# Kernel tuning notes

Hardware: AMD Instinct MI355X
Metric: run time of the kernel (lower is better)

## Reference

```python
import jax, jax.numpy as jnp
import numpy as np

N, IN_DIM, OUT_DIM = 8192, 1024, 1024

def setup_inputs() -> dict:
    key = jax.random.key(0)
    k1, k2, k3, k4 = jax.random.split(key, 4)
    return {
        "input_feature": jax.random.normal(k1, (N, IN_DIM), dtype=jnp.float32),
        "wq": jax.random.normal(k2, (IN_DIM, OUT_DIM), dtype=jnp.float32),
        "wk": jax.random.normal(k3, (IN_DIM, OUT_DIM), dtype=jnp.float32),
        "wv": jax.random.normal(k4, (IN_DIM, OUT_DIM), dtype=jnp.float32),
    }

def reference(input_feature, wq, wk, wv):
    # QKV projections: [N, out_dim]
    q = input_feature @ wq
    k = input_feature @ wk
    v = input_feature @ wv
    # Attention scores [N, N]; note: original applies NO 1/sqrt(d) scaling
    scores = q @ k.T
    attn = jax.nn.softmax(scores, axis=1)
    return attn @ v
```

## Files before the change

### kernel.cpp

```cpp
#include <hip/hip_runtime.h>
#include <hip/hip_bf16.h>
#include <math.h>

#define NROWS 8192
#define DIM   1024
#define CAP   256
#define MARGIN 120.0f

using f16x8 = __attribute__((ext_vector_type(8))) _Float16;
using f32x4 = __attribute__((ext_vector_type(4))) float;
typedef unsigned short u16;
typedef unsigned int   u32;

#define AS1 __attribute__((address_space(1)))
#define AS3 __attribute__((address_space(3)))

__global__ __launch_bounds__(256) void split2h(const float* __restrict__ X,
                                               u16* __restrict__ H,
                                               u16* __restrict__ L) {
    const int idx = (blockIdx.x * 256 + threadIdx.x) * 4;
    float4 x = *(const float4*)&X[idx];
    float c[4] = {x.x, x.y, x.z, x.w};
    u16 h[4], l[4];
#pragma unroll
    for (int i = 0; i < 4; ++i) {
        _Float16 hh = (_Float16)c[i];
        float r = c[i] - (float)hh;
        _Float16 ll = (_Float16)r;
        h[i] = *(u16*)&hh; l[i] = *(u16*)&ll;
    }
    *(ushort4*)&H[idx] = make_ushort4(h[0], h[1], h[2], h[3]);
    *(ushort4*)&L[idx] = make_ushort4(l[0], l[1], l[2], l[3]);
}

__global__ __launch_bounds__(256) void split_wvt(const float* __restrict__ W,
                                                 u16* __restrict__ H) {
    __shared__ float t[64][65];
    const int k0 = blockIdx.x * 64, n0 = blockIdx.y * 64;
    const int c = threadIdx.x & 63, r4 = threadIdx.x >> 6;
#pragma unroll
    for (int i = 0; i < 16; ++i) {
        int k = r4 + i * 4;
        t[k][c] = W[(size_t)(k0 + k) * DIM + n0 + c];
    }
    __syncthreads();
#pragma unroll
    for (int i = 0; i < 16; ++i) {
        int n = r4 + i * 4;
        _Float16 hb = (_Float16)t[c][n];
        H[(n0 + n) * DIM + k0 + c] = *(u16*)&hb;
    }
}

template<int NP>
__device__ __forceinline__ void gemm_lds(const u16* const (&Ap)[NP],
                                         const u16* const (&Bp)[NP],
                                         int row0, int col0, f32x4 (&acc)[4][4],
                                         short (&As)[2][2][4096], short (&Bs)[2][2][4096]) {
    const int tid = threadIdx.x;
    const int w = tid >> 6, lane = tid & 63;
    const int wy = w >> 1, wx = w & 1;
    const int quad = lane >> 4, r16 = lane & 15;

    const int    srow   = w * 32 + (lane >> 2);
    const int    schunk = (lane & 3) * 8;
    const size_t gA0 = (size_t)(row0 + srow) * DIM + schunk;
    const size_t gA1 = gA0 + (size_t)16 * DIM;
    const size_t gB0 = (size_t)(col0 + srow) * DIM + schunk;
    const size_t gB1 = gB0 + (size_t)16 * DIM;
    const int lds0 = (w * 32) * 32;
    const int lds1 = (w * 32 + 16) * 32;

    auto issue = [&](const u16* A, const u16* B, size_t k0, int buf) {
#pragma unroll
        for (int s = 0; s < 2; ++s) {
            const size_t ko = k0 + (size_t)s * 32;
            __builtin_amdgcn_global_load_lds((const AS1 u32*)(A + gA0 + ko), (AS3 u32*)&As[buf][s][lds0], 16, 0, 0);
            __builtin_amdgcn_global_load_lds((const AS1 u32*)(A + gA1 + ko), (AS3 u32*)&As[buf][s][lds1], 16, 0, 0);
            __builtin_amdgcn_global_load_lds((const AS1 u32*)(B + gB0 + ko), (AS3 u32*)&Bs[buf][s][lds0], 16, 0, 0);
            __builtin_amdgcn_global_load_lds((const AS1 u32*)(B + gB1 + ko), (AS3 u32*)&Bs[buf][s][lds1], 16, 0, 0);
        }
    };

    issue(Ap[0], Bp[0], 0, 0);

    int pp = 0;
#pragma unroll
    for (int p = 0; p < NP; ++p) {
        const u16* A = Ap[p];
        const u16* B = Bp[p];
        const u16* An = (p + 1 < NP) ? Ap[p + 1] : A;
        const u16* Bn = (p + 1 < NP) ? Bp[p + 1] : B;
        const bool more = (p + 1 < NP);
        for (int i = 0; i < 16; ++i) {
            __syncthreads();
            const int cur = pp, nxt = pp ^ 1;
            if (i < 15)      issue(A, B, (size_t)(i + 1) * 64, nxt);
            else if (more)   issue(An, Bn, 0, nxt);
#pragma unroll
            for (int s = 0; s < 2; ++s) {
                const short* AsC = As[cur][s];
                const short* BsC = Bs[cur][s];
                f16x8 af[4], bfr[4];
#pragma unroll
                for (int m = 0; m < 4; ++m)
                    af[m] = *(const f16x8*)&AsC[(wy * 64 + m * 16 + r16) * 32 + quad * 8];
#pragma unroll
                for (int n = 0; n < 4; ++n)
                    bfr[n] = *(const f16x8*)&BsC[(wx * 64 + n * 16 + r16) * 32 + quad * 8];
#pragma unroll
                for (int m = 0; m < 4; ++m)
#pragma unroll
                    for (int n = 0; n < 4; ++n)
                        acc[m][n] = __builtin_amdgcn_mfma_f32_16x16x32_f16(af[m], bfr[n], acc[m][n], 0, 0, 0);
            }
            pp ^= 1;
        }
    }
}

__global__ __launch_bounds__(256) void g_gemm(const u16* __restrict__ Wkh, const u16* __restrict__ Wkl,
                                              const u16* __restrict__ Wqh, const u16* __restrict__ Wql,
                                              float* __restrict__ Gt) {
    __shared__ short As[2][2][4096], Bs[2][2][4096];
    const int tid = threadIdx.x, w = tid >> 6, lane = tid & 63;
    const int wy = w >> 1, wx = w & 1, quad = lane >> 4, r16 = lane & 15;
    const int row0 = blockIdx.y * 128, col0 = blockIdx.x * 128;
    const u16* const Ap[3] = { Wkl, Wkh, Wkh };
    const u16* const Bp[3] = { Wqh, Wql, Wqh };
    f32x4 acc[4][4] = {};
    gemm_lds<3>(Ap, Bp, row0, col0, acc, As, Bs);
#pragma unroll
    for (int m = 0; m < 4; ++m)
#pragma unroll
        for (int n = 0; n < 4; ++n)
#pragma unroll
            for (int reg = 0; reg < 4; ++reg) {
                const int row = row0 + wy * 64 + m * 16 + quad * 4 + reg;
                const int col = col0 + wx * 64 + n * 16 + r16;
                Gt[row * DIM + col] = acc[m][n][reg];
            }
}

__global__ __launch_bounds__(256) void yv_gemm(const u16* __restrict__ Xh, const u16* __restrict__ Xl,
                                               const u16* __restrict__ Gth, const u16* __restrict__ Gtl,
                                               const u16* __restrict__ Wvth,
                                               float* __restrict__ Y, u16* __restrict__ Yh, u16* __restrict__ Vh) {
    __shared__ short As[2][2][4096], Bs[2][2][4096];
    const int tid = threadIdx.x, w = tid >> 6, lane = tid & 63;
    const int wy = w >> 1, wx = w & 1, quad = lane >> 4, r16 = lane & 15;
    const int id = blockIdx.x;
    const int z = id >> 9;
    const int within = id & 511;
    const int colt = within >> 6;
    const int rowt = within & 63;
    const int row0 = rowt * 128, col0 = colt * 128;
    f32x4 acc[4][4] = {};
    if (z == 0) {
        const u16* const Ap[3] = { Xl,  Xh,  Xh  };
        const u16* const Bp[3] = { Gth, Gtl, Gth };
        gemm_lds<3>(Ap, Bp, row0, col0, acc, As, Bs);
#pragma unroll
        for (int m = 0; m < 4; ++m)
#pragma unroll
            for (int n = 0; n < 4; ++n)
#pragma unroll
                for (int reg = 0; reg < 4; ++reg) {
                    const int row = row0 + wy * 64 + m * 16 + quad * 4 + reg;
                    const int col = col0 + wx * 64 + n * 16 + r16;
                    float v = acc[m][n][reg];
                    Y[row * DIM + col] = v;
                    _Float16 hb = (_Float16)v;
                    Yh[row * DIM + col] = *(u16*)&hb;
                }
    } else {
        const u16* const Ap[1] = { Xh };
        const u16* const Bp[1] = { Wvth };
        gemm_lds<1>(Ap, Bp, row0, col0, acc, As, Bs);
#pragma unroll
        for (int m = 0; m < 4; ++m)
#pragma unroll
            for (int n = 0; n < 4; ++n)
#pragma unroll
                for (int reg = 0; reg < 4; ++reg) {
                    const int row = row0 + wy * 64 + m * 16 + quad * 4 + reg;
                    const int col = col0 + wx * 64 + n * 16 + r16;
                    _Float16 hb = (_Float16)acc[m][n][reg];
                    Vh[row * DIM + col] = *(u16*)&hb;
                }
    }
}

__global__ __launch_bounds__(256) void filter_kernel(const u16* __restrict__ Yhp,
                                                     const u16* __restrict__ Xhp,
                                                     int* __restrict__ cnt,
                                                     int2* __restrict__ cand) {
    __shared__ short As[2][2][4096], Bs[2][2][4096];
    const int tid = threadIdx.x, w = tid >> 6, lane = tid & 63;
    const int wy = w >> 1, wx = w & 1, quad = lane >> 4, r16 = lane & 15;
    const int id = blockIdx.x;
    const int colt = id >> 6;
    const int rowt = id & 63;
    const int row0 = rowt * 128, col0 = colt * 128;

    const u16* const Ap[1] = { Yhp };
    const u16* const Bp[1] = { Xhp };
    f32x4 acc[4][4] = {};
    gemm_lds<1>(Ap, Bp, row0, col0, acc, As, Bs);

#pragma unroll
    for (int m = 0; m < 4; ++m) {
#pragma unroll
        for (int reg = 0; reg < 4; ++reg) {
            float mx = fmaxf(fmaxf(acc[m][0][reg], acc[m][1][reg]),
                             fmaxf(acc[m][2][reg], acc[m][3][reg]));
            mx = fmaxf(mx, __shfl_xor(mx, 1, 64));
            mx = fmaxf(mx, __shfl_xor(mx, 2, 64));
            mx = fmaxf(mx, __shfl_xor(mx, 4, 64));
            mx = fmaxf(mx, __shfl_xor(mx, 8, 64));
            const float th = mx - MARGIN;
            const int row = row0 + wy * 64 + m * 16 + quad * 4 + reg;
#pragma unroll
            for (int n = 0; n < 4; ++n) {
                float s = acc[m][n][reg];
                if (s >= th) {
                    int pos = atomicAdd(&cnt[row], 1);
                    if (pos < CAP)
                        cand[(size_t)row * CAP + pos] =
                            make_int2(col0 + wx * 64 + n * 16 + r16, __float_as_int(s));
                }
            }
        }
    }
}

__global__ __launch_bounds__(256) void finalize_kernel(const float* __restrict__ Y,
                                                       const float* __restrict__ X,
                                                       const u16* __restrict__ Vh,
                                                       const int* __restrict__ cnt,
                                                       const int2* __restrict__ cand,
                                                       float* __restrict__ out) {
    const int i = blockIdx.x;
    const int tid = threadIdx.x;
    const int w = tid >> 6, lane = tid & 63;
    __shared__ float  red[256];
    __shared__ int    surv[64];
    __shared__ double sprec[64];
    __shared__ float  wgt[64];
    __shared__ int    nsurv;

    const int c = min(cnt[i], CAP);
    float m = -3.0e38f;
    for (int t = tid; t < c; t += 256)
        m = fmaxf(m, __int_as_float(cand[(size_t)i * CAP + t].y));
    red[tid] = m;
    __syncthreads();
    for (int s = 128; s > 0; s >>= 1) {
        if (tid < s) red[tid] = fmaxf(red[tid], red[tid + s]);
        __syncthreads();
    }
    const float th = red[0] - MARGIN;
    if (tid == 0) nsurv = 0;
    __syncthreads();
    for (int t = tid; t < c; t += 256) {
        int2 e = cand[(size_t)i * CAP + t];
        if (__int_as_float(e.y) >= th) {
            int p = atomicAdd(&nsurv, 1);
            if (p < 64) surv[p] = e.x;
        }
    }
    __syncthreads();
    const int ns = min(nsurv, 64);
    for (int u = w; u < ns; u += 4) {
        const int j = surv[u];
        double a = 0.0;
        for (int d = lane; d < DIM; d += 64)
            a += (double)Y[(size_t)i * DIM + d] * (double)X[(size_t)j * DIM + d];
#pragma unroll
        for (int o = 32; o > 0; o >>= 1)
            a += __shfl_down(a, o, 64);
        if (lane == 0) sprec[u] = a;
    }
    __syncthreads();
    if (tid == 0) {
        double mm = -1.0e300;
        for (int u = 0; u < ns; ++u) mm = fmax(mm, sprec[u]);
        double l = 0.0;
        for (int u = 0; u < ns; ++u) l += exp(sprec[u] - mm);
        for (int u = 0; u < ns; ++u) wgt[u] = (float)(exp(sprec[u] - mm) / l);
    }
    __syncthreads();
    for (int d = tid; d < DIM; d += 256) {
        float o = 0.f;
        for (int u = 0; u < ns; ++u) {
            _Float16 hv = *(const _Float16*)&Vh[(size_t)surv[u] * DIM + d];
            o += wgt[u] * (float)hv;
        }
        out[(size_t)i * DIM + d] = o;
    }
}

extern "C" void kernel_launch(void* const* d_in, const int* in_sizes, int n_in,
                              void* d_out, int out_size, void* d_ws, size_t ws_size,
                              hipStream_t stream) {
    const float* X  = (const float*)d_in[0];
    const float* wq = (const float*)d_in[1];
    const float* wk = (const float*)d_in[2];
    const float* wv = (const float*)d_in[3];
    float* out = (float*)d_out;

    char* ws = (char*)d_ws;
    const size_t MB = 1024 * 1024;
    u16*   Xh   = (u16*)(ws +   0 * MB);
    u16*   Xl   = (u16*)(ws +  16 * MB);
    u16*   Wqh  = (u16*)(ws +  32 * MB);
    u16*   Wql  = (u16*)(ws +  34 * MB);
    u16*   Wkh  = (u16*)(ws +  36 * MB);
    u16*   Wkl  = (u16*)(ws +  38 * MB);
    u16*   Wvth = (u16*)(ws +  40 * MB);
    float* Gt   = (float*)(ws + 42 * MB);
    u16*   Gth  = (u16*)(ws +  46 * MB);
    u16*   Gtl  = (u16*)(ws +  48 * MB);
    float* Y    = (float*)(ws + 64 * MB);
    u16*   Yh   = (u16*)(ws +  96 * MB);
    u16*   Vh   = (u16*)(ws + 112 * MB);
    int*   cnt  = (int*)(ws + 128 * MB);
    int2*  cand = (int2*)(ws + 129 * MB);

    hipMemsetAsync(cnt, 0, (size_t)NROWS * 4, stream);

    split2h<<<NROWS * DIM / 1024, 256, 0, stream>>>(X, Xh, Xl);
    split2h<<<DIM * DIM / 1024, 256, 0, stream>>>(wq, Wqh, Wql);
    split2h<<<DIM * DIM / 1024, 256, 0, stream>>>(wk, Wkh, Wkl);
    split_wvt<<<dim3(16, 16), 256, 0, stream>>>(wv, Wvth);

    g_gemm<<<dim3(8, 8), 256, 0, stream>>>(Wkh, Wkl, Wqh, Wql, Gt);
    split2h<<<DIM * DIM / 1024, 256, 0, stream>>>(Gt, Gth, Gtl);

    yv_gemm<<<1024, 256, 0, stream>>>(Xh, Xl, Gth, Gtl, Wvth, Y, Yh, Vh);

    filter_kernel<<<4096, 256, 0, stream>>>(Yh, Xh, cnt, cand);

    finalize_kernel<<<NROWS, 256, 0, stream>>>(Y, X, Vh, cnt, cand, out);
}
```

Baseline: 645.4 us.

## Use 256x256 tiles with 4-stage async LDS pipeline for main GEMMs

```diff
diff --git a/kernel.cpp b/kernel.cpp
--- a/kernel.cpp
+++ b/kernel.cpp
@@ -119,6 +119,79 @@
     }
 }
 
+template<int NP>
+__device__ __forceinline__ void gemm256(const u16* const (&Ap)[NP],
+                                        const u16* const (&Bp)[NP],
+                                        int row0, int col0, f32x4 (&acc)[8][4],
+                                        short (&As)[4][8192], short (&Bs)[4][8192]) {
+    const int tid = threadIdx.x;
+    const int w = tid >> 6, lane = tid & 63;
+    const int wy = w >> 2, wx = w & 3;
+    const int quad = lane >> 4, r16 = lane & 15;
+
+    const int srow   = w * 16 + (lane >> 2);
+    const int schunk = ((lane & 3) ^ ((lane >> 3) & 3)) * 8;
+    const size_t gA0 = (size_t)(row0 + srow) * DIM + schunk;
+    const size_t gA1 = gA0 + (size_t)128 * DIM;
+    const size_t gB0 = (size_t)(col0 + srow) * DIM + schunk;
+    const size_t gB1 = gB0 + (size_t)128 * DIM;
+    const int lds0 = w * 512;
+    const int lds1 = 4096 + w * 512;
+
+    auto stage = [&](int kt, int buf) {
+        const u16* A = Ap[(NP > 1) ? (kt >> 5) : 0];
+        const u16* B = Bp[(NP > 1) ? (kt >> 5) : 0];
+        const size_t ko = (size_t)(kt & 31) * 32;
+        __builtin_amdgcn_global_load_lds((const AS1 u32*)(A + gA0 + ko), (AS3 u32*)&As[buf][lds0], 16, 0, 0);
+        __builtin_amdgcn_global_load_lds((const AS1 u32*)(A + gA1 + ko), (AS3 u32*)&As[buf][lds1], 16, 0, 0);
+        __builtin_amdgcn_global_load_lds((const AS1 u32*)(B + gB0 + ko), (AS3 u32*)&Bs[buf][lds0], 16, 0, 0);
+        __builtin_amdgcn_global_load_lds((const AS1 u32*)(B + gB1 + ko), (AS3 u32*)&Bs[buf][lds1], 16, 0, 0);
+    };
+
+    const int ccol = (quad ^ ((r16 >> 1) & 3)) * 8;
+    const int arow = wy * 128 + r16;
+    const int brow = wx * 64  + r16;
+
+    auto compute = [&](int buf) {
+        f16x8 af[8], bf[4];
+#pragma unroll
+        for (int m = 0; m < 8; ++m)
+            af[m] = *(const f16x8*)&As[buf][(arow + m * 16) * 32 + ccol];
+#pragma unroll
+        for (int n = 0; n < 4; ++n)
+            bf[n] = *(const f16x8*)&Bs[buf][(brow + n * 16) * 32 + ccol];
+        asm volatile("s_waitcnt lgkmcnt(0)" ::: "memory");
+        __builtin_amdgcn_sched_barrier(0);
+        __builtin_amdgcn_s_setprio(1);
+#pragma unroll
+        for (int m = 0; m < 8; ++m)
+#pragma unroll
+            for (int n = 0; n < 4; ++n)
+                acc[m][n] = __builtin_amdgcn_mfma_f32_16x16x32_f16(af[m], bf[n], acc[m][n], 0, 0, 0);
+        __builtin_amdgcn_s_setprio(0);
+        __builtin_amdgcn_sched_barrier(0);
+    };
+
+    constexpr int NK = NP * 32;
+    stage(0, 0); stage(1, 1); stage(2, 2);
+#pragma unroll 1
+    for (int t = 0; t < NK - 2; ++t) {
+        asm volatile("s_waitcnt vmcnt(8)" ::: "memory");
+        __builtin_amdgcn_s_barrier();
+        asm volatile("" ::: "memory");
+        if (t < NK - 3) stage(t + 3, (t + 3) & 3);
+        compute(t & 3);
+    }
+    asm volatile("s_waitcnt vmcnt(4)" ::: "memory");
+    __builtin_amdgcn_s_barrier();
+    asm volatile("" ::: "memory");
+    compute((NK - 2) & 3);
+    asm volatile("s_waitcnt vmcnt(0)" ::: "memory");
+    __builtin_amdgcn_s_barrier();
+    asm volatile("" ::: "memory");
+    compute((NK - 1) & 3);
+}
+
 __global__ __launch_bounds__(256) void g_gemm(const u16* __restrict__ Wkh, const u16* __restrict__ Wkl,
                                               const u16* __restrict__ Wqh, const u16* __restrict__ Wql,
                                               float* __restrict__ Gt) {
@@ -142,74 +215,74 @@
             }
 }
 
-__global__ __launch_bounds__(256) void yv_gemm(const u16* __restrict__ Xh, const u16* __restrict__ Xl,
-                                               const u16* __restrict__ Gth, const u16* __restrict__ Gtl,
-                                               const u16* __restrict__ Wvth,
-                                               float* __restrict__ Y, u16* __restrict__ Yh, u16* __restrict__ Vh) {
-    __shared__ short As[2][2][4096], Bs[2][2][4096];
+__global__ __launch_bounds__(512, 2) void yv_gemm(const u16* __restrict__ Xh, const u16* __restrict__ Xl,
+                                                  const u16* __restrict__ Gth, const u16* __restrict__ Gtl,
+                                                  const u16* __restrict__ Wvth,
+                                                  float* __restrict__ Y, u16* __restrict__ Yh, u16* __restrict__ Vh) {
+    __shared__ short As[4][8192], Bs[4][8192];
     const int tid = threadIdx.x, w = tid >> 6, lane = tid & 63;
-    const int wy = w >> 1, wx = w & 1, quad = lane >> 4, r16 = lane & 15;
+    const int wy = w >> 2, wx = w & 3, quad = lane >> 4, r16 = lane & 15;
     const int id = blockIdx.x;
-    const int z = id >> 9;
-    const int within = id & 511;
-    const int colt = within >> 6;
-    const int rowt = within & 63;
-    const int row0 = rowt * 128, col0 = colt * 128;
-    f32x4 acc[4][4] = {};
-    if (z == 0) {
+    const int part = id >> 7;
+    const int within = id & 127;
+    const int rowt = within >> 2, colt = within & 3;
+    const int row0 = rowt * 256, col0 = colt * 256;
+    f32x4 acc[8][4] = {};
+    if (part == 0) {
         const u16* const Ap[3] = { Xl,  Xh,  Xh  };
         const u16* const Bp[3] = { Gth, Gtl, Gth };
-        gemm_lds<3>(Ap, Bp, row0, col0, acc, As, Bs);
-#pragma unroll
-        for (int m = 0; m < 4; ++m)
+        gemm256<3>(Ap, Bp, row0, col0, acc, As, Bs);
+#pragma unroll
+        for (int m = 0; m < 8; ++m)
 #pragma unroll
             for (int n = 0; n < 4; ++n)
 #pragma unroll
                 for (int reg = 0; reg < 4; ++reg) {
-                    const int row = row0 + wy * 64 + m * 16 + quad * 4 + reg;
+                    const int row = row0 + wy * 128 + m * 16 + quad * 4 + reg;
                     const int col = col0 + wx * 64 + n * 16 + r16;
                     float v = acc[m][n][reg];
-                    Y[row * DIM + col] = v;
+                    Y[(size_t)row * DIM + col] = v;
                     _Float16 hb = (_Float16)v;
-                    Yh[row * DIM + col] = *(u16*)&hb;
+                    Yh[(size_t)row * DIM + col] = *(u16*)&hb;
                 }
     } else {
         const u16* const Ap[1] = { Xh };
         const u16* const Bp[1] = { Wvth };
-        gemm_lds<1>(Ap, Bp, row0, col0, acc, As, Bs);
-#pragma unroll
-        for (int m = 0; m < 4; ++m)
+        gemm256<1>(Ap, Bp, row0, col0, acc, As, Bs);
+#pragma unroll
+        for (int m = 0; m < 8; ++m)
 #pragma unroll
             for (int n = 0; n < 4; ++n)
 #pragma unroll
                 for (int reg = 0; reg < 4; ++reg) {
-                    const int row = row0 + wy * 64 + m * 16 + quad * 4 + reg;
+                    const int row = row0 + wy * 128 + m * 16 + quad * 4 + reg;
                     const int col = col0 + wx * 64 + n * 16 + r16;
                     _Float16 hb = (_Float16)acc[m][n][reg];
-                    Vh[row * DIM + col] = *(u16*)&hb;
+                    Vh[(size_t)row * DIM + col] = *(u16*)&hb;
                 }
     }
 }
 
-__global__ __launch_bounds__(256) void filter_kernel(const u16* __restrict__ Yhp,
-                                                     const u16* __restrict__ Xhp,
-                                                     int* __restrict__ cnt,
-                                                     int2* __restrict__ cand) {
-    __shared__ short As[2][2][4096], Bs[2][2][4096];
+__global__ __launch_bounds__(512, 2) void filter_kernel(const u16* __restrict__ Yhp,
+                                                        const u16* __restrict__ Xhp,
+                                                        int* __restrict__ cnt,
+                                                        int2* __restrict__ cand) {
+    __shared__ short As[4][8192], Bs[4][8192];
     const int tid = threadIdx.x, w = tid >> 6, lane = tid & 63;
-    const int wy = w >> 1, wx = w & 1, quad = lane >> 4, r16 = lane & 15;
+    const int wy = w >> 2, wx = w & 3, quad = lane >> 4, r16 = lane & 15;
     const int id = blockIdx.x;
-    const int colt = id >> 6;
-    const int rowt = id & 63;
-    const int row0 = rowt * 128, col0 = colt * 128;
+    const int xcd = id & 7, within = id >> 3;
+    const int colt = (xcd << 2) | (within & 3);
+    const int rowt = within >> 2;
+    const int row0 = rowt << 8, col0 = colt << 8;
 
     const u16* const Ap[1] = { Yhp };
     const u16* const Bp[1] = { Xhp };
-    f32x4 acc[4][4] = {};
-    gemm_lds<1>(Ap, Bp, row0, col0, acc, As, Bs);
-
-#pragma unroll
-    for (int m = 0; m < 4; ++m) {
+    f32x4 acc[8][4] = {};
+    gemm256<1>(Ap, Bp, row0, col0, acc, As, Bs);
+
+#pragma unroll
+    for (int m = 0; m < 8; ++m) {
 #pragma unroll
         for (int reg = 0; reg < 4; ++reg) {
             float mx = fmaxf(fmaxf(acc[m][0][reg], acc[m][1][reg]),
@@ -219,7 +292,7 @@
             mx = fmaxf(mx, __shfl_xor(mx, 4, 64));
             mx = fmaxf(mx, __shfl_xor(mx, 8, 64));
             const float th = mx - MARGIN;
-            const int row = row0 + wy * 64 + m * 16 + quad * 4 + reg;
+            const int row = row0 + wy * 128 + m * 16 + quad * 4 + reg;
 #pragma unroll
             for (int n = 0; n < 4; ++n) {
                 float s = acc[m][n][reg];
@@ -337,9 +410,9 @@
     g_gemm<<<dim3(8, 8), 256, 0, stream>>>(Wkh, Wkl, Wqh, Wql, Gt);
     split2h<<<DIM * DIM / 1024, 256, 0, stream>>>(Gt, Gth, Gtl);
 
-    yv_gemm<<<1024, 256, 0, stream>>>(Xh, Xl, Gth, Gtl, Wvth, Y, Yh, Vh);
-
-    filter_kernel<<<4096, 256, 0, stream>>>(Yh, Xh, cnt, cand);
+    yv_gemm<<<256, 512, 0, stream>>>(Xh, Xl, Gth, Gtl, Wvth, Y, Yh, Vh);
+
+    filter_kernel<<<1024, 512, 0, stream>>>(Yh, Xh, cnt, cand);
 
     finalize_kernel<<<NROWS, 256, 0, stream>>>(Y, X, Vh, cnt, cand, out);
 }
```

Measured after the change: 721.3 us. 1.12x slower.

## Swizzle LDS tile layout and halve K-step per pipeline stage

Applied to the files above, without the earlier changes.

```diff
diff --git a/kernel.cpp b/kernel.cpp
--- a/kernel.cpp
+++ b/kernel.cpp
@@ -56,14 +56,14 @@
 __device__ __forceinline__ void gemm_lds(const u16* const (&Ap)[NP],
                                          const u16* const (&Bp)[NP],
                                          int row0, int col0, f32x4 (&acc)[4][4],
-                                         short (&As)[2][2][4096], short (&Bs)[2][2][4096]) {
+                                         short (&As)[2][4096], short (&Bs)[2][4096]) {
     const int tid = threadIdx.x;
     const int w = tid >> 6, lane = tid & 63;
     const int wy = w >> 1, wx = w & 1;
     const int quad = lane >> 4, r16 = lane & 15;
 
     const int    srow   = w * 32 + (lane >> 2);
-    const int    schunk = (lane & 3) * 8;
+    const int    schunk = ((lane & 3) ^ ((lane >> 3) & 3)) * 8;
     const size_t gA0 = (size_t)(row0 + srow) * DIM + schunk;
     const size_t gA1 = gA0 + (size_t)16 * DIM;
     const size_t gB0 = (size_t)(col0 + srow) * DIM + schunk;
@@ -71,18 +71,16 @@
     const int lds0 = (w * 32) * 32;
     const int lds1 = (w * 32 + 16) * 32;
 
-    auto issue = [&](const u16* A, const u16* B, size_t k0, int buf) {
-#pragma unroll
-        for (int s = 0; s < 2; ++s) {
-            const size_t ko = k0 + (size_t)s * 32;
-            __builtin_amdgcn_global_load_lds((const AS1 u32*)(A + gA0 + ko), (AS3 u32*)&As[buf][s][lds0], 16, 0, 0);
-            __builtin_amdgcn_global_load_lds((const AS1 u32*)(A + gA1 + ko), (AS3 u32*)&As[buf][s][lds1], 16, 0, 0);
-            __builtin_amdgcn_global_load_lds((const AS1 u32*)(B + gB0 + ko), (AS3 u32*)&Bs[buf][s][lds0], 16, 0, 0);
-            __builtin_amdgcn_global_load_lds((const AS1 u32*)(B + gB1 + ko), (AS3 u32*)&Bs[buf][s][lds1], 16, 0, 0);
-        }
+    auto issue = [&](const u16* A, const u16* B, size_t ko, int buf) {
+        __builtin_amdgcn_global_load_lds((const AS1 u32*)(A + gA0 + ko), (AS3 u32*)&As[buf][lds0], 16, 0, 0);
+        __builtin_amdgcn_global_load_lds((const AS1 u32*)(A + gA1 + ko), (AS3 u32*)&As[buf][lds1], 16, 0, 0);
+        __builtin_amdgcn_global_load_lds((const AS1 u32*)(B + gB0 + ko), (AS3 u32*)&Bs[buf][lds0], 16, 0, 0);
+        __builtin_amdgcn_global_load_lds((const AS1 u32*)(B + gB1 + ko), (AS3 u32*)&Bs[buf][lds1], 16, 0, 0);
     };
 
     issue(Ap[0], Bp[0], 0, 0);
+
+    const int ccol = (quad ^ ((r16 >> 1) & 3)) * 8;
 
     int pp = 0;
 #pragma unroll
@@ -92,28 +90,25 @@
         const u16* An = (p + 1 < NP) ? Ap[p + 1] : A;
         const u16* Bn = (p + 1 < NP) ? Bp[p + 1] : B;
         const bool more = (p + 1 < NP);
-        for (int i = 0; i < 16; ++i) {
+        for (int i = 0; i < 32; ++i) {
             __syncthreads();
             const int cur = pp, nxt = pp ^ 1;
-            if (i < 15)      issue(A, B, (size_t)(i + 1) * 64, nxt);
+            if (i < 31)      issue(A, B, (size_t)(i + 1) * 32, nxt);
             else if (more)   issue(An, Bn, 0, nxt);
-#pragma unroll
-            for (int s = 0; s < 2; ++s) {
-                const short* AsC = As[cur][s];
-                const short* BsC = Bs[cur][s];
-                f16x8 af[4], bfr[4];
-#pragma unroll
-                for (int m = 0; m < 4; ++m)
-                    af[m] = *(const f16x8*)&AsC[(wy * 64 + m * 16 + r16) * 32 + quad * 8];
+            const short* AsC = As[cur];
+            const short* BsC = Bs[cur];
+            f16x8 af[4], bfr[4];
+#pragma unroll
+            for (int m = 0; m < 4; ++m)
+                af[m] = *(const f16x8*)&AsC[(wy * 64 + m * 16 + r16) * 32 + ccol];
+#pragma unroll
+            for (int n = 0; n < 4; ++n)
+                bfr[n] = *(const f16x8*)&BsC[(wx * 64 + n * 16 + r16) * 32 + ccol];
+#pragma unroll
+            for (int m = 0; m < 4; ++m)
 #pragma unroll
                 for (int n = 0; n < 4; ++n)
-                    bfr[n] = *(const f16x8*)&BsC[(wx * 64 + n * 16 + r16) * 32 + quad * 8];
-#pragma unroll
-                for (int m = 0; m < 4; ++m)
-#pragma unroll
-                    for (int n = 0; n < 4; ++n)
-                        acc[m][n] = __builtin_amdgcn_mfma_f32_16x16x32_f16(af[m], bfr[n], acc[m][n], 0, 0, 0);
-            }
+                    acc[m][n] = __builtin_amdgcn_mfma_f32_16x16x32_f16(af[m], bfr[n], acc[m][n], 0, 0, 0);
             pp ^= 1;
         }
     }
@@ -122,7 +117,7 @@
 __global__ __launch_bounds__(256) void g_gemm(const u16* __restrict__ Wkh, const u16* __restrict__ Wkl,
                                               const u16* __restrict__ Wqh, const u16* __restrict__ Wql,
                                               float* __restrict__ Gt) {
-    __shared__ short As[2][2][4096], Bs[2][2][4096];
+    __shared__ short As[2][4096], Bs[2][4096];
     const int tid = threadIdx.x, w = tid >> 6, lane = tid & 63;
     const int wy = w >> 1, wx = w & 1, quad = lane >> 4, r16 = lane & 15;
     const int row0 = blockIdx.y * 128, col0 = blockIdx.x * 128;
@@ -146,7 +141,7 @@
                                                const u16* __restrict__ Gth, const u16* __restrict__ Gtl,
                                                const u16* __restrict__ Wvth,
                                                float* __restrict__ Y, u16* __restrict__ Yh, u16* __restrict__ Vh) {
-    __shared__ short As[2][2][4096], Bs[2][2][4096];
+    __shared__ short As[2][4096], Bs[2][4096];
     const int tid = threadIdx.x, w = tid >> 6, lane = tid & 63;
     const int wy = w >> 1, wx = w & 1, quad = lane >> 4, r16 = lane & 15;
     const int id = blockIdx.x;
@@ -195,7 +190,7 @@
                                                      const u16* __restrict__ Xhp,
                                                      int* __restrict__ cnt,
                                                      int2* __restrict__ cand) {
-    __shared__ short As[2][2][4096], Bs[2][2][4096];
+    __shared__ short As[2][4096], Bs[2][4096];
     const int tid = threadIdx.x, w = tid >> 6, lane = tid & 63;
     const int wy = w >> 1, wx = w & 1, quad = lane >> 4, r16 = lane & 15;
     const int id = blockIdx.x;
```

After: 533.4 us. 1.21x faster.
